# Optimization experiments

Hardware: AMD Instinct MI355X
Metric: run time of the kernel (lower is better)

## Reference

```python
import jax, jax.numpy as jnp
import numpy as np

B = 8192
D = 1024
NUM_HEADS = 16
HEAD_DIM = D // NUM_HEADS  # 64; only used as the softmax scale


def setup_inputs() -> dict:
    key = jax.random.key(0)
    ks = jax.random.split(key, 7)
    s = 1.0 / np.sqrt(D)
    return {
        "x": jax.random.normal(ks[0], (B, D), dtype=jnp.float32),
        "Wq": jax.random.normal(ks[1], (D, D), dtype=jnp.float32) * s,
        "bq": jax.random.normal(ks[2], (D,), dtype=jnp.float32) * s,
        "Wk": jax.random.normal(ks[3], (D, D), dtype=jnp.float32) * s,
        "bk": jax.random.normal(ks[4], (D,), dtype=jnp.float32) * s,
        "Wv": jax.random.normal(ks[5], (D, D), dtype=jnp.float32) * s,
        "bv": jax.random.normal(ks[6], (D,), dtype=jnp.float32) * s,
    }


def reference(x, Wq, bq, Wk, bk, Wv, bv):
    # Faithful to the torch module: x is 2D [B, D]; attention is over the batch axis.
    # nn.Linear computes x @ W.T + b
    Q = x @ Wq.T + bq            # [B, D]
    K = x @ Wk.T + bk            # [B, D]
    V = x @ Wv.T + bv            # [B, D]
    scale = 1.0 / jnp.sqrt(jnp.float32(HEAD_DIM))
    energy = (Q @ K.T) * scale   # [B, B]
    attn = jax.nn.softmax(energy, axis=-1)
    out = attn @ V               # [B, D]
    # torch: x.permute(0,1).contiguous().view(B, seq_len, -1) -> [B, D, 1]
    return out.reshape(B, D, 1)
```

## Files before the change

### kernel.cpp

```cpp
#include <hip/hip_runtime.h>
#include <hip/hip_bf16.h>

typedef _Float16 half_t;
typedef _Float16 f16x8 __attribute__((ext_vector_type(8)));
typedef _Float16 f16x4 __attribute__((ext_vector_type(4)));
typedef float f32x4 __attribute__((ext_vector_type(4)));
typedef float f32x16 __attribute__((ext_vector_type(16)));

#define B_ROWS 8192
#define D_DIM  1024

__device__ __forceinline__ void gload_lds16(const void* g, void* l)
{
    __builtin_amdgcn_global_load_lds((const __attribute__((address_space(1))) void*)g,
                                     (__attribute__((address_space(3))) void*)l, 16, 0, 0);
}

__global__ __launch_bounds__(256)
void cvt_f32_f16(const float* __restrict__ in, half_t* __restrict__ out, int n)
{
    int i = (blockIdx.x * 256 + threadIdx.x) * 4;
    int stride = gridDim.x * 256 * 4;
    for (; i < n; i += stride) {
        float4 v = *(const float4*)&in[i];
        f16x4 o;
        o[0] = (half_t)v.x; o[1] = (half_t)v.y; o[2] = (half_t)v.z; o[3] = (half_t)v.w;
        *(f16x4*)&out[i] = o;
    }
}

__global__ __launch_bounds__(256)
void transpose_h(const half_t* __restrict__ in, half_t* __restrict__ out, int R, int C)
{
    __shared__ half_t t[64][65];
    int tilesC = C >> 6;
    int bc = blockIdx.x % tilesC;
    int br = blockIdx.x / tilesC;
    int r0 = br * 64, c0 = bc * 64;
    for (int e = threadIdx.x; e < 64 * 64; e += 256) {
        int r = e >> 6, c = e & 63;
        t[r][c] = in[(size_t)(r0 + r) * C + (c0 + c)];
    }
    __syncthreads();
    for (int e = threadIdx.x; e < 64 * 64; e += 256) {
        int r = e >> 6, c = e & 63;
        out[(size_t)(c0 + r) * R + (r0 + c)] = t[c][r];
    }
}

template<int EPI>
__device__ __forceinline__ void gemm8_core(
    const half_t* __restrict__ A, const half_t* __restrict__ Bm,
    const float* __restrict__ bias, void* __restrict__ Out,
    int lda, int ldb, int ldc, float scale,
    int row0, int col0, int ktile0, int nkt)
{
    __shared__ __align__(16) half_t As[4 * 8192];
    __shared__ __align__(16) half_t Bs[4 * 8192];

    const int tid  = threadIdx.x;
    const int lane = tid & 63;
    const int wid  = tid >> 6;
    const int wr   = wid >> 2;
    const int wcn  = wid & 3;
    const int l31  = lane & 31;
    const int l32  = lane >> 5;

    const int trow  = tid >> 3;
    const int tslot = (tid & 7) ^ (trow & 7);
    const char* Apan[2] = { (const char*)(A + (size_t)row0 * lda),
                            (const char*)(A + (size_t)(row0 + 128) * lda) };
    const char* Bpan[2] = { (const char*)(Bm + (size_t)col0 * ldb),
                            (const char*)(Bm + (size_t)(col0 + 128) * ldb) };
    const size_t aoff[2] = { (size_t)trow * lda * 2 + (size_t)tslot * 16,
                             (size_t)(trow + 64) * lda * 2 + (size_t)tslot * 16 };
    const size_t boff[2] = { (size_t)trow * ldb * 2 + (size_t)tslot * 16,
                             (size_t)(trow + 64) * ldb * 2 + (size_t)tslot * 16 };
    const int dstb[2] = { tid * 16, 8192 + tid * 16 };

    auto stageA = [&](int h, int s, int buf) {
        char* d = (char*)(As + (buf * 2 + h) * 8192);
        const char* g = Apan[h] + (size_t)(ktile0 + s) * 128;
        gload_lds16(g + aoff[0], d + dstb[0]);
        gload_lds16(g + aoff[1], d + dstb[1]);
    };
    auto stageB = [&](int h, int s, int buf) {
        char* d = (char*)(Bs + (buf * 2 + h) * 8192);
        const char* g = Bpan[h] + (size_t)(ktile0 + s) * 128;
        gload_lds16(g + boff[0], d + dstb[0]);
        gload_lds16(g + boff[1], d + dstb[1]);
    };
    auto rdA = [&](int mm, int kc, const half_t* base) -> f16x8 {
        int rih  = wr * 64 + mm * 32 + l31;
        int byte = rih * 128 + (((kc * 2 + l32) ^ (rih & 7)) << 4);
        return *(const f16x8*)((const char*)base + byte);
    };
    auto rdB = [&](int kc, const half_t* base) -> f16x8 {
        int rih  = wcn * 32 + l31;
        int byte = rih * 128 + (((kc * 2 + l32) ^ (rih & 7)) << 4);
        return *(const f16x8*)((const char*)base + byte);
    };

    f32x16 acc[2][2][2] = {};
    f16x8 af[2][4];
    f16x8 bfP[4], bfQ[4];

    stageB(0, 0, 0); stageA(0, 0, 0); stageB(1, 0, 0); stageA(1, 0, 0);
    asm volatile("s_waitcnt vmcnt(6)" ::: "memory");
    asm volatile("s_barrier" ::: "memory");
    {
        const half_t* B0 = Bs;
        #pragma unroll
        for (int kc = 0; kc < 4; ++kc) bfP[kc] = rdB(kc, B0);
    }

    for (int t = 0; t < nkt; ++t) {
        const int buf  = t & 1;
        const int bufn = buf ^ 1;
        const half_t* A0  = As + (buf * 2 + 0) * 8192;
        const half_t* A1  = As + (buf * 2 + 1) * 8192;
        const half_t* B1c = Bs + (buf * 2 + 1) * 8192;
        const half_t* B0n = Bs + (bufn * 2 + 0) * 8192;
        const int t1s = (t + 1 < nkt) ? t + 1 : nkt - 1;

        asm volatile("s_waitcnt vmcnt(2)" ::: "memory");
        asm volatile("s_barrier" ::: "memory");
        #pragma unroll
        for (int kc = 0; kc < 4; ++kc)
            #pragma unroll
            for (int mm = 0; mm < 2; ++mm) af[mm][kc] = rdA(mm, kc, A0);
        #pragma unroll
        for (int kc = 0; kc < 4; ++kc) bfQ[kc] = rdB(kc, B1c);
        stageB(0, t1s, bufn);
        __builtin_amdgcn_s_setprio(1);
        #pragma unroll
        for (int kc = 0; kc < 4; ++kc)
            #pragma unroll
            for (int mm = 0; mm < 2; ++mm)
                acc[0][mm][0] = __builtin_amdgcn_mfma_f32_32x32x16_f16(af[mm][kc], bfP[kc], acc[0][mm][0], 0, 0, 0);
        __builtin_amdgcn_s_setprio(0);

        stageA(0, t1s, bufn);
        __builtin_amdgcn_s_setprio(1);
        #pragma unroll
        for (int kc = 0; kc < 4; ++kc)
            #pragma unroll
            for (int mm = 0; mm < 2; ++mm)
                acc[0][mm][1] = __builtin_amdgcn_mfma_f32_32x32x16_f16(af[mm][kc], bfQ[kc], acc[0][mm][1], 0, 0, 0);
        __builtin_amdgcn_s_setprio(0);

        asm volatile("s_waitcnt vmcnt(4)" ::: "memory");
        asm volatile("s_barrier" ::: "memory");
        #pragma unroll
        for (int kc = 0; kc < 4; ++kc)
            #pragma unroll
            for (int mm = 0; mm < 2; ++mm) af[mm][kc] = rdA(mm, kc, A1);
        stageB(1, t1s, bufn);
        __builtin_amdgcn_s_setprio(1);
        #pragma unroll
        for (int kc = 0; kc < 4; ++kc)
            #pragma unroll
            for (int mm = 0; mm < 2; ++mm)
                acc[1][mm][0] = __builtin_amdgcn_mfma_f32_32x32x16_f16(af[mm][kc], bfP[kc], acc[1][mm][0], 0, 0, 0);
        __builtin_amdgcn_s_setprio(0);

        asm volatile("s_waitcnt vmcnt(4)" ::: "memory");
        asm volatile("s_barrier" ::: "memory");
        #pragma unroll
        for (int kc = 0; kc < 4; ++kc) bfP[kc] = rdB(kc, B0n);
        stageA(1, t1s, bufn);
        __builtin_amdgcn_s_setprio(1);
        #pragma unroll
        for (int kc = 0; kc < 4; ++kc)
            #pragma unroll
            for (int mm = 0; mm < 2; ++mm)
                acc[1][mm][1] = __builtin_amdgcn_mfma_f32_32x32x16_f16(af[mm][kc], bfQ[kc], acc[1][mm][1], 0, 0, 0);
        __builtin_amdgcn_s_setprio(0);
    }

    #pragma unroll
    for (int h = 0; h < 2; ++h) {
        #pragma unroll
        for (int mm = 0; mm < 2; ++mm) {
            int r0 = row0 + h * 128 + wr * 64 + mm * 32 + 4 * l32;
            #pragma unroll
            for (int nh = 0; nh < 2; ++nh) {
                int gcol = col0 + nh * 128 + wcn * 32 + l31;
                float badd = (EPI == 0) ? bias[gcol] : 0.0f;
                #pragma unroll
                for (int g = 0; g < 16; ++g) {
                    int row = r0 + (g & 3) + 8 * (g >> 2);
                    float v = acc[h][mm][nh][g] * scale + badd;
                    size_t idx = (size_t)row * ldc + gcol;
                    if (EPI == 2) ((float*)Out)[idx] = v;
                    else          ((half_t*)Out)[idx] = (half_t)v;
                }
            }
        }
    }
}

template<int EPI, int REMAP>
__global__ __launch_bounds__(512, 2)
void gemm8(const half_t* __restrict__ A, const half_t* __restrict__ Bm,
           const float* __restrict__ bias, void* __restrict__ Out,
           int lda, int ldb, int ldc, float scale, int nkt)
{
    int bx, by;
    if (REMAP) {
        int L = blockIdx.y * gridDim.x + blockIdx.x;
        int s = L >> 8;
        int u = L & 255;
        int xcd  = u & 7;
        int slot = u >> 3;
        by = (s >> 1) * 16 + xcd * 2 + (slot >> 4);
        bx = (s & 1) * 16 + (slot & 15);
    } else {
        int nwg = gridDim.x * gridDim.y;
        int bid = blockIdx.y * gridDim.x + blockIdx.x;
        if ((nwg & 7) == 0) { int c = nwg >> 3; bid = (bid & 7) * c + (bid >> 3); }
        bx = bid % gridDim.x; by = bid / gridDim.x;
    }
    gemm8_core<EPI>(A, Bm, bias, Out, lda, ldb, ldc, scale, by * 256, bx * 256, 0, nkt);
}

__global__ __launch_bounds__(512, 2)
void gemm8_qkv(const half_t* __restrict__ xh,
               const half_t* __restrict__ Wq, const half_t* __restrict__ Wk, const half_t* __restrict__ Wv,
               const float* __restrict__ bq, const float* __restrict__ bk, const float* __restrict__ bv,
               half_t* __restrict__ Q, half_t* __restrict__ K, half_t* __restrict__ V)
{
    int z = blockIdx.z;
    const half_t* W = (z == 0) ? Wq : (z == 1) ? Wk : Wv;
    const float*  b = (z == 0) ? bq : (z == 1) ? bk : bv;
    half_t*       O = (z == 0) ? Q  : (z == 1) ? K  : V;
    gemm8_core<0>(xh, W, b, O, D_DIM, D_DIM, D_DIM, 1.0f,
                  blockIdx.y * 256, blockIdx.x * 256, 0, D_DIM / 64);
}

__global__ __launch_bounds__(512, 2)
void gemm8_pv(const half_t* __restrict__ S, const half_t* __restrict__ Vt,
              float* __restrict__ part0, float* __restrict__ part1)
{
    int h = blockIdx.z * 128 + blockIdx.y * 4 + blockIdx.x;
    int l = (h & 7) * 32 + (h >> 3);
    int z  = l >> 7;
    int r  = l & 127;
    int by = r >> 2;
    int bx = r & 3;
    float* O = z ? part1 : part0;
    gemm8_core<2>(S, Vt, nullptr, O, B_ROWS, B_ROWS, D_DIM, 1.0f,
                  by * 256, bx * 256, z * (B_ROWS / 128), B_ROWS / 128);
}

__global__ __launch_bounds__(256)
void add_f32(const float* __restrict__ a, float* __restrict__ out, int n)
{
    int i = (blockIdx.x * 256 + threadIdx.x) * 4;
    int stride = gridDim.x * 256 * 4;
    for (; i < n; i += stride) {
        float4 x = *(const float4*)&out[i];
        float4 y = *(const float4*)&a[i];
        x.x += y.x; x.y += y.y; x.z += y.z; x.w += y.w;
        *(float4*)&out[i] = x;
    }
}

__global__ __launch_bounds__(256)
void softmax_rows(half_t* __restrict__ S, int ncol)
{
    const int row = blockIdx.x;
    half_t* srow = S + (size_t)row * ncol;
    const int tid = threadIdx.x;

    float ev[32];
    float m = -1e30f;
    #pragma unroll
    for (int it = 0; it < 4; ++it) {
        int j = it * 2048 + tid * 8;
        f16x8 v = *(const f16x8*)&srow[j];
        #pragma unroll
        for (int t = 0; t < 8; ++t) {
            float f = (float)v[t];
            ev[it * 8 + t] = f;
            m = fmaxf(m, f);
        }
    }
    #pragma unroll
    for (int o = 32; o; o >>= 1) m = fmaxf(m, __shfl_down(m, o));
    __shared__ float redm[8];
    __shared__ float reds[8];
    if ((tid & 63) == 0) redm[tid >> 6] = m;
    __syncthreads();
    m = fmaxf(fmaxf(redm[0], redm[1]), fmaxf(redm[2], redm[3]));

    float s = 0.0f;
    #pragma unroll
    for (int e = 0; e < 32; ++e) {
        float ex = __expf(ev[e] - m);
        ev[e] = ex;
        s += ex;
    }
    #pragma unroll
    for (int o = 32; o; o >>= 1) s += __shfl_down(s, o);
    if ((tid & 63) == 0) reds[tid >> 6] = s;
    __syncthreads();
    s = reds[0] + reds[1] + reds[2] + reds[3];
    float inv = 1.0f / s;

    #pragma unroll
    for (int it = 0; it < 4; ++it) {
        int j = it * 2048 + tid * 8;
        f16x8 o8;
        #pragma unroll
        for (int t = 0; t < 8; ++t) o8[t] = (half_t)(ev[it * 8 + t] * inv);
        *(f16x8*)&srow[j] = o8;
    }
}

extern "C" void kernel_launch(void* const* d_in, const int* in_sizes, int n_in,
                              void* d_out, int out_size, void* d_ws, size_t ws_size,
                              hipStream_t stream)
{
    const float* x  = (const float*)d_in[0];
    const float* Wq = (const float*)d_in[1];
    const float* bq = (const float*)d_in[2];
    const float* Wk = (const float*)d_in[3];
    const float* bk = (const float*)d_in[4];
    const float* Wv = (const float*)d_in[5];
    const float* bv = (const float*)d_in[6];
    float* out = (float*)d_out;

    const int Bb = B_ROWS, Dd = D_DIM;

    char* w = (char*)d_ws;
    size_t off = 0;
    auto carve = [&](size_t bytes) {
        void* p = w + off;
        off += (bytes + 255) & ~(size_t)255;
        return p;
    };
    half_t* xh  = (half_t*)carve((size_t)Bb * Dd * 2);
    half_t* Wqh = (half_t*)carve((size_t)Dd * Dd * 2);
    half_t* Wkh = (half_t*)carve((size_t)Dd * Dd * 2);
    half_t* Wvh = (half_t*)carve((size_t)Dd * Dd * 2);
    half_t* Qh  = (half_t*)carve((size_t)Bb * Dd * 2);
    half_t* Kh  = (half_t*)carve((size_t)Bb * Dd * 2);
    half_t* Vh  = (half_t*)carve((size_t)Bb * Dd * 2);
    half_t* S   = (half_t*)carve((size_t)Bb * Bb * 2);
    half_t* Vt  = xh;
    float*  part1 = (float*)Qh;

    cvt_f32_f16<<<2048, 256, 0, stream>>>(x,  xh,  Bb * Dd);
    cvt_f32_f16<<<1024, 256, 0, stream>>>(Wq, Wqh, Dd * Dd);
    cvt_f32_f16<<<1024, 256, 0, stream>>>(Wk, Wkh, Dd * Dd);
    cvt_f32_f16<<<1024, 256, 0, stream>>>(Wv, Wvh, Dd * Dd);

    dim3 gqkv(Dd / 256, Bb / 256, 3);
    gemm8_qkv<<<gqkv, 512, 0, stream>>>(xh, Wqh, Wkh, Wvh, bq, bk, bv, Qh, Kh, Vh);

    transpose_h<<<(Dd / 64) * (Bb / 64), 256, 0, stream>>>(Vh, Vt, Bb, Dd);

    dim3 gs(Bb / 256, Bb / 256);
    gemm8<1, 1><<<gs, 512, 0, stream>>>(Qh, Kh, nullptr, S, Dd, Dd, Bb, 0.125f, Dd / 64);

    softmax_rows<<<Bb, 256, 0, stream>>>(S, Bb);

    dim3 gpv(Dd / 256, Bb / 256, 2);
    gemm8_pv<<<gpv, 512, 0, stream>>>(S, Vt, out, part1);
    add_f32<<<2048, 256, 0, stream>>>(part1, out, Bb * Dd);
}
```

Measured before the change: 458.9 us.

## Ping-pong wave groups in GEMM mainloop with two-tile-deep LDS prefetch

The GEMM main loop is restructured so the two wave rows alternate roles. While one group issues LDS reads and global-to-LDS staging, the other runs its MFMA block, with barriers between each of eight phases. Prefetch depth rises to two tiles ahead: half-0 of tile t+2 is staged into the current buffer, and the prologue preloads part of tile 1. The aim is to hide LDS-read and load-issue latency behind matrix math on the other wave group, at the cost of many more barriers per iteration and a more fragile ordering of vmcnt waits.

```diff
diff --git a/kernel.cpp b/kernel.cpp
--- a/kernel.cpp
+++ b/kernel.cpp
@@ -65,6 +65,7 @@
     const int wcn  = wid & 3;
     const int l31  = lane & 31;
     const int l32  = lane >> 5;
+    const bool g0  = (wr == 0);
 
     const int trow  = tid >> 3;
     const int tslot = (tid & 7) ^ (trow & 7);
@@ -105,78 +106,111 @@
     f16x8 af[2][4];
     f16x8 bfP[4], bfQ[4];
 
-    stageB(0, 0, 0); stageA(0, 0, 0); stageB(1, 0, 0); stageA(1, 0, 0);
-    asm volatile("s_waitcnt vmcnt(6)" ::: "memory");
+    auto M1 = [&]() {
+        __builtin_amdgcn_s_setprio(1);
+        #pragma unroll
+        for (int kc = 0; kc < 4; ++kc)
+            #pragma unroll
+            for (int mm = 0; mm < 2; ++mm)
+                acc[0][mm][0] = __builtin_amdgcn_mfma_f32_32x32x16_f16(af[mm][kc], bfP[kc], acc[0][mm][0], 0, 0, 0);
+        __builtin_amdgcn_s_setprio(0);
+    };
+    auto M2 = [&]() {
+        __builtin_amdgcn_s_setprio(1);
+        #pragma unroll
+        for (int kc = 0; kc < 4; ++kc)
+            #pragma unroll
+            for (int mm = 0; mm < 2; ++mm)
+                acc[0][mm][1] = __builtin_amdgcn_mfma_f32_32x32x16_f16(af[mm][kc], bfQ[kc], acc[0][mm][1], 0, 0, 0);
+        __builtin_amdgcn_s_setprio(0);
+    };
+    auto M3 = [&]() {
+        __builtin_amdgcn_s_setprio(1);
+        #pragma unroll
+        for (int kc = 0; kc < 4; ++kc)
+            #pragma unroll
+            for (int mm = 0; mm < 2; ++mm)
+                acc[1][mm][0] = __builtin_amdgcn_mfma_f32_32x32x16_f16(af[mm][kc], bfP[kc], acc[1][mm][0], 0, 0, 0);
+        __builtin_amdgcn_s_setprio(0);
+    };
+    auto M4 = [&]() {
+        __builtin_amdgcn_s_setprio(1);
+        #pragma unroll
+        for (int kc = 0; kc < 4; ++kc)
+            #pragma unroll
+            for (int mm = 0; mm < 2; ++mm)
+                acc[1][mm][1] = __builtin_amdgcn_mfma_f32_32x32x16_f16(af[mm][kc], bfQ[kc], acc[1][mm][1], 0, 0, 0);
+        __builtin_amdgcn_s_setprio(0);
+    };
+
+    {
+        int s1 = (nkt > 1) ? 1 : 0;
+        stageA(0, 0, 0); stageB(0, 0, 0); stageA(1, 0, 0); stageB(1, 0, 0);
+        stageA(0, s1, 1); stageB(0, s1, 1);
+    }
+    asm volatile("s_waitcnt vmcnt(4)" ::: "memory");
     asm volatile("s_barrier" ::: "memory");
-    {
-        const half_t* B0 = Bs;
-        #pragma unroll
-        for (int kc = 0; kc < 4; ++kc) bfP[kc] = rdB(kc, B0);
-    }
-
+
+    #define BAR asm volatile("s_barrier" ::: "memory")
     for (int t = 0; t < nkt; ++t) {
         const int buf  = t & 1;
         const int bufn = buf ^ 1;
         const half_t* A0  = As + (buf * 2 + 0) * 8192;
         const half_t* A1  = As + (buf * 2 + 1) * 8192;
+        const half_t* B0c = Bs + (buf * 2 + 0) * 8192;
         const half_t* B1c = Bs + (buf * 2 + 1) * 8192;
         const half_t* B0n = Bs + (bufn * 2 + 0) * 8192;
         const int t1s = (t + 1 < nkt) ? t + 1 : nkt - 1;
-
-        asm volatile("s_waitcnt vmcnt(2)" ::: "memory");
-        asm volatile("s_barrier" ::: "memory");
-        #pragma unroll
-        for (int kc = 0; kc < 4; ++kc)
-            #pragma unroll
-            for (int mm = 0; mm < 2; ++mm) af[mm][kc] = rdA(mm, kc, A0);
-        #pragma unroll
-        for (int kc = 0; kc < 4; ++kc) bfQ[kc] = rdB(kc, B1c);
-        stageB(0, t1s, bufn);
-        __builtin_amdgcn_s_setprio(1);
-        #pragma unroll
-        for (int kc = 0; kc < 4; ++kc)
-            #pragma unroll
-            for (int mm = 0; mm < 2; ++mm)
-                acc[0][mm][0] = __builtin_amdgcn_mfma_f32_32x32x16_f16(af[mm][kc], bfP[kc], acc[0][mm][0], 0, 0, 0);
-        __builtin_amdgcn_s_setprio(0);
-
-        stageA(0, t1s, bufn);
-        __builtin_amdgcn_s_setprio(1);
-        #pragma unroll
-        for (int kc = 0; kc < 4; ++kc)
-            #pragma unroll
-            for (int mm = 0; mm < 2; ++mm)
-                acc[0][mm][1] = __builtin_amdgcn_mfma_f32_32x32x16_f16(af[mm][kc], bfQ[kc], acc[0][mm][1], 0, 0, 0);
-        __builtin_amdgcn_s_setprio(0);
-
-        asm volatile("s_waitcnt vmcnt(4)" ::: "memory");
-        asm volatile("s_barrier" ::: "memory");
-        #pragma unroll
-        for (int kc = 0; kc < 4; ++kc)
-            #pragma unroll
-            for (int mm = 0; mm < 2; ++mm) af[mm][kc] = rdA(mm, kc, A1);
-        stageB(1, t1s, bufn);
-        __builtin_amdgcn_s_setprio(1);
-        #pragma unroll
-        for (int kc = 0; kc < 4; ++kc)
-            #pragma unroll
-            for (int mm = 0; mm < 2; ++mm)
-                acc[1][mm][0] = __builtin_amdgcn_mfma_f32_32x32x16_f16(af[mm][kc], bfP[kc], acc[1][mm][0], 0, 0, 0);
-        __builtin_amdgcn_s_setprio(0);
-
-        asm volatile("s_waitcnt vmcnt(4)" ::: "memory");
-        asm volatile("s_barrier" ::: "memory");
-        #pragma unroll
-        for (int kc = 0; kc < 4; ++kc) bfP[kc] = rdB(kc, B0n);
-        stageA(1, t1s, bufn);
-        __builtin_amdgcn_s_setprio(1);
-        #pragma unroll
-        for (int kc = 0; kc < 4; ++kc)
-            #pragma unroll
-            for (int mm = 0; mm < 2; ++mm)
-                acc[1][mm][1] = __builtin_amdgcn_mfma_f32_32x32x16_f16(af[mm][kc], bfQ[kc], acc[1][mm][1], 0, 0, 0);
-        __builtin_amdgcn_s_setprio(0);
-    }
+        const int t2s = (t + 2 < nkt) ? t + 2 : nkt - 1;
+
+        auto R1 = [&]() {
+            #pragma unroll
+            for (int kc = 0; kc < 4; ++kc)
+                #pragma unroll
+                for (int mm = 0; mm < 2; ++mm) af[mm][kc] = rdA(mm, kc, A0);
+            #pragma unroll
+            for (int kc = 0; kc < 4; ++kc) bfP[kc] = rdB(kc, B0c);
+        };
+        auto R2 = [&]() {
+            #pragma unroll
+            for (int kc = 0; kc < 4; ++kc) bfQ[kc] = rdB(kc, B1c);
+        };
+        auto R3 = [&]() {
+            #pragma unroll
+            for (int kc = 0; kc < 4; ++kc)
+                #pragma unroll
+                for (int mm = 0; mm < 2; ++mm) af[mm][kc] = rdA(mm, kc, A1);
+        };
+        auto R4 = [&]() {
+            #pragma unroll
+            for (int kc = 0; kc < 4; ++kc) bfP[kc] = rdB(kc, B0n);
+        };
+        auto S1 = [&]() { stageA(1, t1s, bufn); };
+        auto S2 = [&]() { stageB(1, t1s, bufn); };
+        auto S3 = [&]() { stageA(0, t2s, buf); };
+        auto S4 = [&]() { stageB(0, t2s, buf); };
+
+        if (g0) { asm volatile("s_waitcnt vmcnt(4)" ::: "memory"); R1(); S1(); }
+        else if (t > 0) { M4(); }
+        BAR;
+        if (g0) { M1(); }
+        else { asm volatile("s_waitcnt vmcnt(4)" ::: "memory"); R1(); S1(); }
+        BAR;
+        if (g0) { R2(); S2(); } else { M1(); }
+        BAR;
+        if (g0) { M2(); } else { R2(); S2(); }
+        BAR;
+        if (g0) { R3(); S3(); } else { M2(); }
+        BAR;
+        if (g0) { M3(); } else { R3(); S3(); }
+        BAR;
+        if (g0) { R4(); S4(); } else { M3(); }
+        BAR;
+        if (g0) { M4(); } else { R4(); S4(); }
+        BAR;
+    }
+    #undef BAR
+    if (!g0) { M4(); }
 
     #pragma unroll
     for (int h = 0; h < 2; ++h) {
```

Result: slower. 500.0 us (+9.0%).
